# Kernel tuning notes

Hardware: AMD Instinct MI355X
Metric: run time of the kernel (lower is better)

## Reference

```python
import jax, jax.numpy as jnp
import numpy as np

B, L, D, H, KV = 2, 2048, 2048, 16, 4
K = D // H  # head dim = 128
ROPE_BASE = 10000.0


def _rope_tables(seq_len, dim):
    inv_freq = 1.0 / (ROPE_BASE ** (jnp.arange(0, dim, 2, dtype=jnp.float32) / dim))
    t = jnp.arange(seq_len, dtype=jnp.float32)
    freqs = jnp.outer(t, inv_freq)  # [L, dim/2]
    return jnp.cos(freqs), jnp.sin(freqs)


def _apply_rope(x, cos, sin):
    # x: [B, h, L, K]; interleaved-pair rotation, matching torch stack+flatten
    x1 = x[..., ::2]
    x2 = x[..., 1::2]
    c = cos[None, None, :, :]
    s = sin[None, None, :, :]
    o1 = x1 * c - x2 * s
    o2 = x1 * s + x2 * c
    return jnp.stack((o1, o2), axis=-1).reshape(x.shape)


def setup_inputs() -> dict:
    key = jax.random.key(0)
    ks = jax.random.split(key, 5)
    scale = D ** -0.5
    return {
        "x": jax.random.normal(ks[0], (B, L, D), jnp.float32),
        "wq": jax.random.normal(ks[1], (D, D), jnp.float32) * scale,
        "wk": jax.random.normal(ks[2], (KV * K, D), jnp.float32) * scale,
        "wv": jax.random.normal(ks[3], (KV * K, D), jnp.float32) * scale,
        "wo": jax.random.normal(ks[4], (D, D), jnp.float32) * scale,
    }


def reference(x, wq, wk, wv, wo):
    Bx, Lx, Dx = x.shape
    # projections (nn.Linear: y = x @ W.T)
    q = (x @ wq.T).reshape(Bx, Lx, H, K).transpose(0, 2, 1, 3)   # [B,H,L,K]
    k = (x @ wk.T).reshape(Bx, Lx, KV, K).transpose(0, 2, 1, 3)  # [B,KV,L,K]
    v = (x @ wv.T).reshape(Bx, Lx, KV, K).transpose(0, 2, 1, 3)
    cos, sin = _rope_tables(Lx, K)
    q = _apply_rope(q, cos, sin)
    k = _apply_rope(k, cos, sin)
    # GQA: repeat_interleave KV heads to H heads
    rep = H // KV
    k = jnp.repeat(k, rep, axis=1)
    v = jnp.repeat(v, rep, axis=1)
    scores = jnp.einsum('bhqd,bhkd->bhqk', q, k) / jnp.sqrt(jnp.float32(K))
    causal = jnp.tril(jnp.ones((Lx, Lx), dtype=bool))
    scores = jnp.where(causal[None, None], scores, jnp.finfo(scores.dtype).min)
    attn = jax.nn.softmax(scores, axis=-1)
    out = jnp.einsum('bhqk,bhkd->bhqd', attn, v)
    out = out.transpose(0, 2, 1, 3).reshape(Bx, Lx, Dx)
    return out @ wo.T
```

## Files before the change

### kernel.cpp

```cpp
#include <hip/hip_runtime.h>
#include <stdint.h>

#define DEV static __device__ __forceinline__

typedef __attribute__((ext_vector_type(8))) short s16x8;
typedef __attribute__((ext_vector_type(4))) short s16x4;
typedef __attribute__((ext_vector_type(4))) float f32x4;

constexpr int BB = 2, LL = 2048, DD = 2048, NH = 16, NKV = 4, HD = 128;
constexpr int Mrows = BB * LL;
constexpr int NQKV = DD + 2 * NKV * HD;

DEV ushort f2bf(float f){
  union { float f; uint32_t u; } v; v.f = f;
  uint32_t u = v.u;
  u += 0x7fffu + ((u >> 16) & 1u);
  return (ushort)(u >> 16);
}
DEV float bf2f(ushort h){
  union { uint32_t u; float f; } v; v.u = ((uint32_t)h) << 16;
  return v.f;
}

DEV f32x4 mfma32(s16x8 a, s16x8 b, f32x4 c){
  return __builtin_amdgcn_mfma_f32_16x16x32_bf16(a, b, c, 0, 0, 0);
}
DEV f32x4 mfma16(s16x4 a, s16x4 b, f32x4 c){
#if __has_builtin(__builtin_amdgcn_mfma_f32_16x16x16bf16_1k)
  return __builtin_amdgcn_mfma_f32_16x16x16bf16_1k(a, b, c, 0, 0, 0);
#else
  asm volatile("v_mfma_f32_16x16x16_bf16 %0, %1, %2, %0" : "+v"(c) : "v"(a), "v"(b));
  return c;
#endif
}

DEV float vmax4(f32x4 v){ return fmaxf(fmaxf(v[0], v[1]), fmaxf(v[2], v[3])); }
DEV float vsum4(f32x4 v){ return (v[0] + v[1]) + (v[2] + v[3]); }

__global__ void cvt_all_kernel(const float* __restrict__ x, const float* __restrict__ wq,
                               const float* __restrict__ wk, const float* __restrict__ wv,
                               const float* __restrict__ wo,
                               ushort* __restrict__ xb, ushort* __restrict__ wqkv,
                               ushort* __restrict__ wob){
  constexpr int C0 = Mrows * DD / 4;
  constexpr int C1 = C0 + DD * DD / 4;
  constexpr int C2 = C1 + NKV * HD * DD / 4;
  constexpr int C3 = C2 + NKV * HD * DD / 4;
  constexpr int C4 = C3 + DD * DD / 4;
  int stride = gridDim.x * blockDim.x;
  for (int i = blockIdx.x * blockDim.x + threadIdx.x; i < C4; i += stride){
    const float* src; ushort* dst; int j;
    if (i < C0){ src = x;  dst = xb;                              j = i; }
    else if (i < C1){ src = wq; dst = wqkv;                       j = i - C0; }
    else if (i < C2){ src = wk; dst = wqkv + (size_t)DD * DD;     j = i - C1; }
    else if (i < C3){ src = wv; dst = wqkv + (size_t)(DD + NKV*HD) * DD; j = i - C2; }
    else { src = wo; dst = wob;                                   j = i - C3; }
    float4 v = reinterpret_cast<const float4*>(src)[j];
    ushort4 o = make_ushort4(f2bf(v.x), f2bf(v.y), f2bf(v.z), f2bf(v.w));
    reinterpret_cast<ushort4*>(dst)[j] = o;
  }
}

__global__ void rope_table_kernel(float* __restrict__ cosT, float* __restrict__ sinT){
  int i = blockIdx.x * blockDim.x + threadIdx.x;
  if (i >= LL * 64) return;
  int l = i >> 6, f = i & 63;
  float inv = __expf(-logf(10000.f) * (float)f / 64.f);
  float ang = (float)l * inv;
  float s, c;
  sincosf(ang, &s, &c);
  cosT[i] = c; sinT[i] = s;
}

__global__ void rope_qk_kernel(ushort* __restrict__ q, ushort* __restrict__ k,
                               const float* __restrict__ cosT, const float* __restrict__ sinT){
  constexpr int TQ = BB * NH * LL * 16;
  constexpr int TK = BB * NKV * LL * 16;
  int idx = blockIdx.x * blockDim.x + threadIdx.x;
  if (idx >= TQ + TK) return;
  ushort* t; float scale; int id;
  if (idx < TQ){ t = q; id = idx; scale = 0.08838834764831845f; }
  else { t = k; id = idx - TQ; scale = 1.0f; }
  int c = id & 15;
  int l = (id >> 4) & (LL - 1);
  s16x8 v = *reinterpret_cast<const s16x8*>(t + (size_t)id * 8);
  int fb = (l << 6) + c * 4;
  s16x8 o;
  #pragma unroll
  for (int j = 0; j < 4; ++j){
    float x1 = bf2f((ushort)v[2*j]);
    float x2 = bf2f((ushort)v[2*j+1]);
    float co = cosT[fb + j], si = sinT[fb + j];
    o[2*j]   = (short)f2bf((x1 * co - x2 * si) * scale);
    o[2*j+1] = (short)f2bf((x1 * si + x2 * co) * scale);
  }
  *reinterpret_cast<s16x8*>(t + (size_t)id * 8) = o;
}

DEV void g2l16(const void* g, void* l){
  __builtin_amdgcn_global_load_lds((__attribute__((address_space(1))) void*)(void*)g,
                                   (__attribute__((address_space(3))) void*)l, 16, 0, 0);
}

__global__ __launch_bounds__(256) void gemm_qkv_kernel(const ushort* __restrict__ A,
    const ushort* __restrict__ W, ushort* __restrict__ qo, ushort* __restrict__ ko,
    ushort* __restrict__ vo)
{
  __shared__ ushort Asm[128 * 32];
  __shared__ ushort Bsm[128 * 32];
  const int tid = threadIdx.x;
  const int lane = tid & 63;
  const int wr = tid >> 7;
  const int wc = (tid >> 6) & 1;
  const int lr = lane & 15, lg = lane >> 4;
  const int brow = blockIdx.y * 128, bcol = blockIdx.x * 128;

  f32x4 acc[4][4] = {};

  for (int kb = 0; kb < DD; kb += 32){
    #pragma unroll
    for (int it = 0; it < 2; ++it){
      int seg = it * 256 + tid;
      int row = seg >> 2, sc = seg & 3;
      g2l16(A + (size_t)(brow + row) * DD + kb + sc * 8, &Asm[seg * 8]);
    }
    #pragma unroll
    for (int it = 0; it < 2; ++it){
      int seg = it * 256 + tid;
      int row = seg >> 2, sc = seg & 3;
      g2l16(W + (size_t)(bcol + row) * DD + kb + sc * 8, &Bsm[seg * 8]);
    }
    __syncthreads();
    s16x8 af[4], bfr[4];
    #pragma unroll
    for (int m = 0; m < 4; ++m)
      af[m] = *reinterpret_cast<const s16x8*>(&Asm[(wr*64 + m*16 + lr)*32 + lg*8]);
    #pragma unroll
    for (int n = 0; n < 4; ++n)
      bfr[n] = *reinterpret_cast<const s16x8*>(&Bsm[(wc*64 + n*16 + lr)*32 + lg*8]);
    #pragma unroll
    for (int m = 0; m < 4; ++m)
      #pragma unroll
      for (int n = 0; n < 4; ++n)
        acc[m][n] = mfma32(af[m], bfr[n], acc[m][n]);
    __syncthreads();
  }

  #pragma unroll
  for (int m = 0; m < 4; ++m)
    #pragma unroll
    for (int n = 0; n < 4; ++n)
      #pragma unroll
      for (int r = 0; r < 4; ++r){
        int row = brow + wr*64 + m*16 + lg*4 + r;
        int col = bcol + wc*64 + n*16 + lr;
        int b = row >> 11, l = row & (LL - 1);
        ushort bv = f2bf(acc[m][n][r]);
        if (col < DD){
          qo[(((size_t)(b * NH + (col >> 7))) * LL + l) * HD + (col & 127)] = bv;
        } else if (col < DD + NKV * HD){
          int c = col - DD;
          ko[(((size_t)(b * NKV + (c >> 7))) * LL + l) * HD + (c & 127)] = bv;
        } else {
          int c = col - DD - NKV * HD;
          vo[(((size_t)(b * NKV + (c >> 7))) * HD + (c & 127)) * LL + l] = bv;
        }
      }
}

__global__ __launch_bounds__(256) void gemm_o_kernel(const ushort* __restrict__ A,
    const ushort* __restrict__ W, float* __restrict__ outp)
{
  __shared__ ushort Asm[128 * 32];
  __shared__ ushort Bsm[128 * 32];
  const int tid = threadIdx.x;
  const int lane = tid & 63;
  const int wr = tid >> 7;
  const int wc = (tid >> 6) & 1;
  const int lr = lane & 15, lg = lane >> 4;
  const int brow = blockIdx.y * 128, bcol = blockIdx.x * 128;

  f32x4 acc[4][4] = {};

  for (int kb = 0; kb < DD; kb += 32){
    #pragma unroll
    for (int it = 0; it < 2; ++it){
      int seg = it * 256 + tid;
      int row = seg >> 2, sc = seg & 3;
      g2l16(A + (size_t)(brow + row) * DD + kb + sc * 8, &Asm[seg * 8]);
    }
    #pragma unroll
    for (int it = 0; it < 2; ++it){
      int seg = it * 256 + tid;
      int row = seg >> 2, sc = seg & 3;
      g2l16(W + (size_t)(bcol + row) * DD + kb + sc * 8, &Bsm[seg * 8]);
    }
    __syncthreads();
    s16x8 af[4], bfr[4];
    #pragma unroll
    for (int m = 0; m < 4; ++m)
      af[m] = *reinterpret_cast<const s16x8*>(&Asm[(wr*64 + m*16 + lr)*32 + lg*8]);
    #pragma unroll
    for (int n = 0; n < 4; ++n)
      bfr[n] = *reinterpret_cast<const s16x8*>(&Bsm[(wc*64 + n*16 + lr)*32 + lg*8]);
    #pragma unroll
    for (int m = 0; m < 4; ++m)
      #pragma unroll
      for (int n = 0; n < 4; ++n)
        acc[m][n] = mfma32(af[m], bfr[n], acc[m][n]);
    __syncthreads();
  }

  #pragma unroll
  for (int m = 0; m < 4; ++m)
    #pragma unroll
    for (int n = 0; n < 4; ++n)
      #pragma unroll
      for (int r = 0; r < 4; ++r){
        int row = brow + wr*64 + m*16 + lg*4 + r;
        int col = bcol + wc*64 + n*16 + lr;
        outp[(size_t)row * DD + col] = acc[m][n][r];
      }
}

__global__ __launch_bounds__(256) void attn_kernel(const ushort* __restrict__ Q,
    const ushort* __restrict__ Kg, const ushort* __restrict__ VTg, ushort* __restrict__ O)
{
  __shared__ ushort Ksm[2][64 * 128];
  __shared__ ushort Vsm[2][128 * 64];
  const int tid = threadIdx.x;
  const int w = tid >> 6, lane = tid & 63;
  const int lr = lane & 15, lg = lane >> 4;
  const int bh = blockIdx.y;
  const int b = bh >> 4, h = bh & 15, kvh = h >> 2;
  const int qbb = b ? (int)blockIdx.x : ((int)gridDim.x - 1 - (int)blockIdx.x);
  const size_t qoff = (size_t)bh * LL * HD;
  const size_t koff = (size_t)(b * NKV + kvh) * LL * HD;
  const size_t voff = (size_t)(b * NKV + kvh) * HD * LL;
  const int qb0 = qbb * 128;
  const int qrow0 = qb0 + w * 32;
  const int wlast = qrow0 + 31;

  s16x8 qf[2][4];
  #pragma unroll
  for (int qt = 0; qt < 2; ++qt)
    #pragma unroll
    for (int kk = 0; kk < 4; ++kk)
      qf[qt][kk] = *reinterpret_cast<const s16x8*>(
          &Q[qoff + (size_t)(qrow0 + qt*16 + lr) * HD + kk*32 + lg*8]);

  f32x4 of[2][8] = {};
  float mrun[2] = {-1e30f, -1e30f}, lrun[2] = {0.f, 0.f};

  const int nt = 2 * qbb + 2;

  auto STAGE = [&](int buf, int jb){
    #pragma unroll
    for (int it = 0; it < 4; ++it){
      int chunk = it * 256 + tid;
      int r = chunk >> 4, c = chunk & 15;
      g2l16(Kg + koff + (size_t)(jb + r) * HD + ((c ^ (r & 7)) << 3), &Ksm[buf][chunk << 3]);
    }
    #pragma unroll
    for (int it = 0; it < 4; ++it){
      int chunk = it * 256 + tid;
      int r = chunk >> 3, c = chunk & 7;
      g2l16(VTg + voff + (size_t)r * LL + jb + ((c ^ (r & 7)) << 3), &Vsm[buf][chunk << 3]);
    }
  };
  STAGE(0, 0);

  for (int t = 0; t < nt; ++t){
    const int jb = t << 6, cur = t & 1;
    __syncthreads();
    if (t + 1 < nt) STAGE(cur ^ 1, (t + 1) << 6);
    if (jb <= wlast){
      f32x4 s[4][2] = {};
      __builtin_amdgcn_s_setprio(1);
      #pragma unroll
      for (int kk = 0; kk < 4; ++kk)
        #pragma unroll
        for (int kt = 0; kt < 4; ++kt){
          s16x8 kf = *reinterpret_cast<const s16x8*>(
              &Ksm[cur][((kt*16 + lr) << 7) + (((kk*4 + lg) ^ (lr & 7)) << 3)]);
          s[kt][0] = mfma32(kf, qf[0][kk], s[kt][0]);
          s[kt][1] = mfma32(kf, qf[1][kk], s[kt][1]);
        }
      __builtin_amdgcn_s_setprio(0);
      if (jb + 63 > qrow0){
        #pragma unroll
        for (int kt = 0; kt < 4; ++kt){
          int kvg = jb + kt*16 + lg*4;
          #pragma unroll
          for (int qt = 0; qt < 2; ++qt){
            int qg = qrow0 + qt*16 + lr;
            #pragma unroll
            for (int r = 0; r < 4; ++r)
              if (kvg + r > qg) s[kt][qt][r] = -1e30f;
          }
        }
      }
      float mx[2];
      #pragma unroll
      for (int qt = 0; qt < 2; ++qt){
        mx[qt] = fmaxf(fmaxf(vmax4(s[0][qt]), vmax4(s[1][qt])),
                       fmaxf(vmax4(s[2][qt]), vmax4(s[3][qt])));
        mx[qt] = fmaxf(mx[qt], __shfl_xor(mx[qt], 16, 64));
        mx[qt] = fmaxf(mx[qt], __shfl_xor(mx[qt], 32, 64));
      }
      int small = (mx[0] <= mrun[0] + 8.f) && (mx[1] <= mrun[1] + 8.f);
      if (!__all(small)){
        float mn0 = fmaxf(mrun[0], mx[0]), mn1 = fmaxf(mrun[1], mx[1]);
        float fac0 = __expf(mrun[0] - mn0), fac1 = __expf(mrun[1] - mn1);
        mrun[0] = mn0; mrun[1] = mn1;
        lrun[0] *= fac0; lrun[1] *= fac1;
        #pragma unroll
        for (int f = 0; f < 8; ++f){ of[0][f] *= fac0; of[1][f] *= fac1; }
      }
      float ps[2] = {0.f, 0.f};
      #pragma unroll
      for (int kt = 0; kt < 4; ++kt)
        #pragma unroll
        for (int qt = 0; qt < 2; ++qt){
          #pragma unroll
          for (int r = 0; r < 4; ++r)
            s[kt][qt][r] = __expf(s[kt][qt][r] - mrun[qt]);
          ps[qt] += vsum4(s[kt][qt]);
        }
      #pragma unroll
      for (int qt = 0; qt < 2; ++qt){
        ps[qt] += __shfl_xor(ps[qt], 16, 64);
        ps[qt] += __shfl_xor(ps[qt], 32, 64);
        lrun[qt] += ps[qt];
      }
      s16x4 pb[4][2];
      #pragma unroll
      for (int kt = 0; kt < 4; ++kt)
        #pragma unroll
        for (int qt = 0; qt < 2; ++qt){
          s16x4 pv;
          #pragma unroll
          for (int r = 0; r < 4; ++r) pv[r] = (short)f2bf(s[kt][qt][r]);
          pb[kt][qt] = pv;
        }
      __builtin_amdgcn_s_setprio(1);
      #pragma unroll
      for (int f = 0; f < 8; ++f)
        #pragma unroll
        for (int kt = 0; kt < 4; ++kt){
          s16x4 va = *reinterpret_cast<const s16x4*>(
              &Vsm[cur][((f*16 + lr) << 6) + (((2*kt + (lg >> 1)) ^ (lr & 7)) << 3) + ((lg & 1) << 2)]);
          of[0][f] = mfma16(va, pb[kt][0], of[0][f]);
          of[1][f] = mfma16(va, pb[kt][1], of[1][f]);
        }
      __builtin_amdgcn_s_setprio(0);
    }
  }

  #pragma unroll
  for (int qt = 0; qt < 2; ++qt){
    float inv = 1.0f / lrun[qt];
    #pragma unroll
    for (int f = 0; f < 8; ++f)
      #pragma unroll
      for (int r = 0; r < 4; ++r){
        int row = qrow0 + qt*16 + lr;
        int col = h * HD + f*16 + lg*4 + r;
        O[((size_t)b * LL + row) * DD + col] = f2bf(of[qt][f][r] * inv);
      }
  }
}

extern "C" void kernel_launch(void* const* d_in, const int* in_sizes, int n_in,
                              void* d_out, int out_size, void* d_ws, size_t ws_size,
                              hipStream_t stream)
{
  const float* x  = (const float*)d_in[0];
  const float* wq = (const float*)d_in[1];
  const float* wk = (const float*)d_in[2];
  const float* wv = (const float*)d_in[3];
  const float* wo = (const float*)d_in[4];
  float* out = (float*)d_out;

  char* p = (char*)d_ws;
  auto alloc = [&](size_t bytes) -> void* {
    void* r = (void*)p; p += (bytes + 255) & ~(size_t)255; return r;
  };
  ushort* xb    = (ushort*)alloc((size_t)Mrows * DD * 2);
  ushort* wqkvb = (ushort*)alloc((size_t)NQKV * DD * 2);
  ushort* wob   = (ushort*)alloc((size_t)DD * DD * 2);
  ushort* qws   = (ushort*)alloc((size_t)BB * NH * LL * HD * 2);
  ushort* kws   = (ushort*)alloc((size_t)BB * NKV * LL * HD * 2);
  ushort* vws   = (ushort*)alloc((size_t)BB * NKV * LL * HD * 2);
  ushort* aows  = (ushort*)alloc((size_t)Mrows * DD * 2);
  float*  cosT  = (float*)alloc((size_t)LL * 64 * 4);
  float*  sinT  = (float*)alloc((size_t)LL * 64 * 4);

  hipLaunchKernelGGL(cvt_all_kernel, dim3(2048), dim3(256), 0, stream,
                     x, wq, wk, wv, wo, xb, wqkvb, wob);
  hipLaunchKernelGGL(rope_table_kernel, dim3((LL*64)/256), dim3(256), 0, stream, cosT, sinT);

  hipLaunchKernelGGL(gemm_qkv_kernel, dim3(NQKV/128, Mrows/128), dim3(256), 0, stream,
                     xb, wqkvb, qws, kws, vws);

  {
    constexpr int tot = BB*NH*LL*16 + BB*NKV*LL*16;
    hipLaunchKernelGGL(rope_qk_kernel, dim3(tot/256), dim3(256), 0, stream,
                       qws, kws, cosT, sinT);
  }

  hipLaunchKernelGGL(attn_kernel, dim3(LL/128, BB*NH), dim3(256), 0, stream,
                     qws, kws, vws, aows);

  hipLaunchKernelGGL(gemm_o_kernel, dim3(DD/128, Mrows/128), dim3(256), 0, stream,
                     aows, wob, out);
}
```

Before: 403.1 us.

## Pair causal query tiles per block and remap grids for XCD locality

The attention kernel now gives each block two 64-row query strips from opposite ends of the sequence (pair and 31-pair), so every block does a balanced amount of causal work. The shared K/V tiles are reused for both strips while both are active, and only the later strip runs after that. All three GEMM/attention grids become 1D with an id remapping ((id&7)*N + id>>3), so that blocks sharing operands land on the same XCD and reuse its L2. The cost is more complex indexing, and each wave now holds 16 query rows per strip instead of 32 contiguous rows, which changes the MFMA work each wave does per K/V tile.

```diff
diff --git a/kernel.cpp b/kernel.cpp
--- a/kernel.cpp
+++ b/kernel.cpp
@@ -113,7 +113,11 @@
   const int wr = tid >> 7;
   const int wc = (tid >> 6) & 1;
   const int lr = lane & 15, lg = lane >> 4;
-  const int brow = blockIdx.y * 128, bcol = blockIdx.x * 128;
+  const int id = blockIdx.x;
+  const int nid = (id & 7) * 96 + (id >> 3);
+  const int bx = nid >> 5;
+  const int by = nid & 31;
+  const int brow = by * 128, bcol = bx * 128;
 
   f32x4 acc[4][4] = {};
 
@@ -178,7 +182,11 @@
   const int wr = tid >> 7;
   const int wc = (tid >> 6) & 1;
   const int lr = lane & 15, lg = lane >> 4;
-  const int brow = blockIdx.y * 128, bcol = blockIdx.x * 128;
+  const int id = blockIdx.x;
+  const int nid = (id & 7) * 64 + (id >> 3);
+  const int bx = nid >> 5;
+  const int by = nid & 31;
+  const int brow = by * 128, bcol = bx * 128;
 
   f32x4 acc[4][4] = {};
 
@@ -221,6 +229,107 @@
         int col = bcol + wc*64 + n*16 + lr;
         outp[(size_t)row * DD + col] = acc[m][n][r];
       }
+}
+
+template<int NQ>
+DEV void tile_step(const ushort* __restrict__ Ks, const ushort* __restrict__ Vs,
+                   const s16x8 (*qf)[4], f32x4 (*of)[8], float* mrun, float* lrun,
+                   const int* qrow, int jb, int lr, int lg)
+{
+  f32x4 s[4][NQ];
+  #pragma unroll
+  for (int kt = 0; kt < 4; ++kt)
+    #pragma unroll
+    for (int q = 0; q < NQ; ++q) s[kt][q] = (f32x4){0.f, 0.f, 0.f, 0.f};
+
+  __builtin_amdgcn_s_setprio(1);
+  #pragma unroll
+  for (int kk = 0; kk < 4; ++kk)
+    #pragma unroll
+    for (int kt = 0; kt < 4; ++kt){
+      s16x8 kf = *reinterpret_cast<const s16x8*>(
+          &Ks[((kt*16 + lr) << 7) + (((kk*4 + lg) ^ (lr & 7)) << 3)]);
+      #pragma unroll
+      for (int q = 0; q < NQ; ++q)
+        s[kt][q] = mfma32(kf, qf[q][kk], s[kt][q]);
+    }
+  __builtin_amdgcn_s_setprio(0);
+
+  #pragma unroll
+  for (int q = 0; q < NQ; ++q)
+    if (jb + 63 > qrow[q]){
+      int qg = qrow[q] + lr;
+      #pragma unroll
+      for (int kt = 0; kt < 4; ++kt){
+        int kvg = jb + kt*16 + lg*4;
+        #pragma unroll
+        for (int r = 0; r < 4; ++r)
+          if (kvg + r > qg) s[kt][q][r] = -1e30f;
+      }
+    }
+
+  float mx[NQ];
+  #pragma unroll
+  for (int q = 0; q < NQ; ++q){
+    mx[q] = fmaxf(fmaxf(vmax4(s[0][q]), vmax4(s[1][q])),
+                  fmaxf(vmax4(s[2][q]), vmax4(s[3][q])));
+    mx[q] = fmaxf(mx[q], __shfl_xor(mx[q], 16, 64));
+    mx[q] = fmaxf(mx[q], __shfl_xor(mx[q], 32, 64));
+  }
+  int small = 1;
+  #pragma unroll
+  for (int q = 0; q < NQ; ++q) small &= (mx[q] <= mrun[q] + 8.f);
+  if (!__all(small)){
+    #pragma unroll
+    for (int q = 0; q < NQ; ++q){
+      float mn = fmaxf(mrun[q], mx[q]);
+      float fac = __expf(mrun[q] - mn);
+      mrun[q] = mn;
+      lrun[q] *= fac;
+      #pragma unroll
+      for (int f = 0; f < 8; ++f) of[q][f] *= fac;
+    }
+  }
+  float ps[NQ];
+  #pragma unroll
+  for (int q = 0; q < NQ; ++q) ps[q] = 0.f;
+  #pragma unroll
+  for (int kt = 0; kt < 4; ++kt)
+    #pragma unroll
+    for (int q = 0; q < NQ; ++q){
+      #pragma unroll
+      for (int r = 0; r < 4; ++r)
+        s[kt][q][r] = __expf(s[kt][q][r] - mrun[q]);
+      ps[q] += vsum4(s[kt][q]);
+    }
+  #pragma unroll
+  for (int q = 0; q < NQ; ++q){
+    ps[q] += __shfl_xor(ps[q], 16, 64);
+    ps[q] += __shfl_xor(ps[q], 32, 64);
+    lrun[q] += ps[q];
+  }
+  s16x4 pb[4][NQ];
+  #pragma unroll
+  for (int kt = 0; kt < 4; ++kt)
+    #pragma unroll
+    for (int q = 0; q < NQ; ++q){
+      s16x4 pv;
+      #pragma unroll
+      for (int r = 0; r < 4; ++r) pv[r] = (short)f2bf(s[kt][q][r]);
+      pb[kt][q] = pv;
+    }
+  __builtin_amdgcn_s_setprio(1);
+  #pragma unroll
+  for (int f = 0; f < 8; ++f)
+    #pragma unroll
+    for (int kt = 0; kt < 4; ++kt){
+      s16x4 va = *reinterpret_cast<const s16x4*>(
+          &Vs[((f*16 + lr) << 6) + (((2*kt + (lg >> 1)) ^ (lr & 7)) << 3) + ((lg & 1) << 2)]);
+      #pragma unroll
+      for (int q = 0; q < NQ; ++q)
+        of[q][f] = mfma16(va, pb[kt][q], of[q][f]);
+    }
+  __builtin_amdgcn_s_setprio(0);
 }
 
 __global__ __launch_bounds__(256) void attn_kernel(const ushort* __restrict__ Q,
@@ -231,15 +340,17 @@
   const int tid = threadIdx.x;
   const int w = tid >> 6, lane = tid & 63;
   const int lr = lane & 15, lg = lane >> 4;
-  const int bh = blockIdx.y;
+  const int id = blockIdx.x;
+  const int nid = (id & 7) * 64 + (id >> 3);
+  const int pair = nid & 15;
+  const int bh = nid >> 4;
   const int b = bh >> 4, h = bh & 15, kvh = h >> 2;
-  const int qbb = b ? (int)blockIdx.x : ((int)gridDim.x - 1 - (int)blockIdx.x);
   const size_t qoff = (size_t)bh * LL * HD;
   const size_t koff = (size_t)(b * NKV + kvh) * LL * HD;
   const size_t voff = (size_t)(b * NKV + kvh) * HD * LL;
-  const int qb0 = qbb * 128;
-  const int qrow0 = qb0 + w * 32;
-  const int wlast = qrow0 + 31;
+  const int qrow[2] = { pair*64 + w*16, (31 - pair)*64 + w*16 };
+  const int nt  = 32 - pair;
+  const int ntA = pair + 1;
 
   s16x8 qf[2][4];
   #pragma unroll
@@ -247,12 +358,10 @@
     #pragma unroll
     for (int kk = 0; kk < 4; ++kk)
       qf[qt][kk] = *reinterpret_cast<const s16x8*>(
-          &Q[qoff + (size_t)(qrow0 + qt*16 + lr) * HD + kk*32 + lg*8]);
+          &Q[qoff + (size_t)(qrow[qt] + lr) * HD + kk*32 + lg*8]);
 
   f32x4 of[2][8] = {};
   float mrun[2] = {-1e30f, -1e30f}, lrun[2] = {0.f, 0.f};
-
-  const int nt = 2 * qbb + 2;
 
   auto STAGE = [&](int buf, int jb){
     #pragma unroll
@@ -274,87 +383,10 @@
     const int jb = t << 6, cur = t & 1;
     __syncthreads();
     if (t + 1 < nt) STAGE(cur ^ 1, (t + 1) << 6);
-    if (jb <= wlast){
-      f32x4 s[4][2] = {};
-      __builtin_amdgcn_s_setprio(1);
-      #pragma unroll
-      for (int kk = 0; kk < 4; ++kk)
-        #pragma unroll
-        for (int kt = 0; kt < 4; ++kt){
-          s16x8 kf = *reinterpret_cast<const s16x8*>(
-              &Ksm[cur][((kt*16 + lr) << 7) + (((kk*4 + lg) ^ (lr & 7)) << 3)]);
-          s[kt][0] = mfma32(kf, qf[0][kk], s[kt][0]);
-          s[kt][1] = mfma32(kf, qf[1][kk], s[kt][1]);
-        }
-      __builtin_amdgcn_s_setprio(0);
-      if (jb + 63 > qrow0){
-        #pragma unroll
-        for (int kt = 0; kt < 4; ++kt){
-          int kvg = jb + kt*16 + lg*4;
-          #pragma unroll
-          for (int qt = 0; qt < 2; ++qt){
-            int qg = qrow0 + qt*16 + lr;
-            #pragma unroll
-            for (int r = 0; r < 4; ++r)
-              if (kvg + r > qg) s[kt][qt][r] = -1e30f;
-          }
-        }
-      }
-      float mx[2];
-      #pragma unroll
-      for (int qt = 0; qt < 2; ++qt){
-        mx[qt] = fmaxf(fmaxf(vmax4(s[0][qt]), vmax4(s[1][qt])),
-                       fmaxf(vmax4(s[2][qt]), vmax4(s[3][qt])));
-        mx[qt] = fmaxf(mx[qt], __shfl_xor(mx[qt], 16, 64));
-        mx[qt] = fmaxf(mx[qt], __shfl_xor(mx[qt], 32, 64));
-      }
-      int small = (mx[0] <= mrun[0] + 8.f) && (mx[1] <= mrun[1] + 8.f);
-      if (!__all(small)){
-        float mn0 = fmaxf(mrun[0], mx[0]), mn1 = fmaxf(mrun[1], mx[1]);
-        float fac0 = __expf(mrun[0] - mn0), fac1 = __expf(mrun[1] - mn1);
-        mrun[0] = mn0; mrun[1] = mn1;
-        lrun[0] *= fac0; lrun[1] *= fac1;
-        #pragma unroll
-        for (int f = 0; f < 8; ++f){ of[0][f] *= fac0; of[1][f] *= fac1; }
-      }
-      float ps[2] = {0.f, 0.f};
-      #pragma unroll
-      for (int kt = 0; kt < 4; ++kt)
-        #pragma unroll
-        for (int qt = 0; qt < 2; ++qt){
-          #pragma unroll
-          for (int r = 0; r < 4; ++r)
-            s[kt][qt][r] = __expf(s[kt][qt][r] - mrun[qt]);
-          ps[qt] += vsum4(s[kt][qt]);
-        }
-      #pragma unroll
-      for (int qt = 0; qt < 2; ++qt){
-        ps[qt] += __shfl_xor(ps[qt], 16, 64);
-        ps[qt] += __shfl_xor(ps[qt], 32, 64);
-        lrun[qt] += ps[qt];
-      }
-      s16x4 pb[4][2];
-      #pragma unroll
-      for (int kt = 0; kt < 4; ++kt)
-        #pragma unroll
-        for (int qt = 0; qt < 2; ++qt){
-          s16x4 pv;
-          #pragma unroll
-          for (int r = 0; r < 4; ++r) pv[r] = (short)f2bf(s[kt][qt][r]);
-          pb[kt][qt] = pv;
-        }
-      __builtin_amdgcn_s_setprio(1);
-      #pragma unroll
-      for (int f = 0; f < 8; ++f)
-        #pragma unroll
-        for (int kt = 0; kt < 4; ++kt){
-          s16x4 va = *reinterpret_cast<const s16x4*>(
-              &Vsm[cur][((f*16 + lr) << 6) + (((2*kt + (lg >> 1)) ^ (lr & 7)) << 3) + ((lg & 1) << 2)]);
-          of[0][f] = mfma16(va, pb[kt][0], of[0][f]);
-          of[1][f] = mfma16(va, pb[kt][1], of[1][f]);
-        }
-      __builtin_amdgcn_s_setprio(0);
-    }
+    if (t < ntA)
+      tile_step<2>(Ksm[cur], Vsm[cur], qf, of, mrun, lrun, qrow, jb, lr, lg);
+    else
+      tile_step<1>(Ksm[cur], Vsm[cur], qf + 1, of + 1, mrun + 1, lrun + 1, qrow + 1, jb, lr, lg);
   }
 
   #pragma unroll
@@ -364,7 +396,7 @@
     for (int f = 0; f < 8; ++f)
       #pragma unroll
       for (int r = 0; r < 4; ++r){
-        int row = qrow0 + qt*16 + lr;
+        int row = qrow[qt] + lr;
         int col = h * HD + f*16 + lg*4 + r;
         O[((size_t)b * LL + row) * DD + col] = f2bf(of[qt][f][r] * inv);
       }
@@ -400,7 +432,7 @@
                      x, wq, wk, wv, wo, xb, wqkvb, wob);
   hipLaunchKernelGGL(rope_table_kernel, dim3((LL*64)/256), dim3(256), 0, stream, cosT, sinT);
 
-  hipLaunchKernelGGL(gemm_qkv_kernel, dim3(NQKV/128, Mrows/128), dim3(256), 0, stream,
+  hipLaunchKernelGGL(gemm_qkv_kernel, dim3(768), dim3(256), 0, stream,
                      xb, wqkvb, qws, kws, vws);
 
   {
@@ -409,9 +441,9 @@
                        qws, kws, cosT, sinT);
   }
 
-  hipLaunchKernelGGL(attn_kernel, dim3(LL/128, BB*NH), dim3(256), 0, stream,
+  hipLaunchKernelGGL(attn_kernel, dim3(512), dim3(256), 0, stream,
                      qws, kws, vws, aows);
 
-  hipLaunchKernelGGL(gemm_o_kernel, dim3(DD/128, Mrows/128), dim3(256), 0, stream,
+  hipLaunchKernelGGL(gemm_o_kernel, dim3(512), dim3(256), 0, stream,
                      aows, wob, out);
 }
```

Measured after the change: 397.0 us. Within noise of the previous version (-1.5%).
